# Performance work log

Hardware: AMD Instinct MI355X
Metric: run time of the kernel (lower is better)

Reference implementation:

```python
import jax, jax.numpy as jnp
import numpy as np

B, T, C = 4, 2048, 768
H, N = 12, 64
N_LAYER, LAYER_ID = 12, 1
EPS_GN = 0.00064


def setup_inputs():
    key = jax.random.key(0)
    ks = jax.random.split(key, 20)
    r01 = LAYER_ID / (N_LAYER - 1)
    r10 = 1.0 - LAYER_ID / N_LAYER
    ddd = (np.arange(C, dtype=np.float64) / C)[None, None, :]

    def lam(p, off=0.0):
        return jnp.asarray(1.0 - np.power(ddd, p) - off, dtype=jnp.float32)

    decay = -7.0 + 5.0 * (np.arange(C, dtype=np.float64) / (C - 1)) ** (0.85 + r01 ** 0.5)

    def rn(i, shape, scale):
        return scale * jax.random.normal(ks[i], shape, jnp.float32)

    s = 1.0 / C ** 0.5
    return {
        "x": jax.random.normal(ks[0], (B, T, C), jnp.float32),
        "v_first": jax.random.normal(ks[1], (B, T, C), jnp.float32),
        "lambda_r": lam(0.2 * r10), "lambda_w": lam(0.9 * r10),
        "lambda_k": lam(0.9 * r10, 0.4 * r01), "lambda_v": lam(0.4 * r10, 0.6 * r01),
        "lambda_a": lam(0.9 * r10), "lambda_g": lam(0.2 * r10),
        "w_miu": jnp.asarray(decay[None, None, :] + 0.5, jnp.float32),
        "w_A": rn(2, (C, 64), 0.02), "w_B": rn(3, (64, C), 0.02),
        "a_miu": jnp.zeros((1, 1, C), jnp.float32),
        "a_A": rn(4, (C, 64), 0.02), "a_B": rn(5, (64, C), 0.02),
        "v_miu": jnp.ones((1, 1, C), jnp.float32),
        "v_A": rn(6, (C, 64), 0.02), "v_B": rn(7, (64, C), 0.02),
        "g_A": rn(8, (C, 128), 0.02), "g_B": rn(9, (128, C), 0.02),
        "k_k": 0.85 * jnp.ones((1, 1, C), jnp.float32),
        "k_a": jnp.ones((1, 1, C), jnp.float32),
        "r_k": rn(10, (H, N), 0.02),
        "W_r": jax.random.uniform(ks[11], (C, C), jnp.float32, -0.5 * s, 0.5 * s),
        "W_k": jax.random.uniform(ks[12], (C, C), jnp.float32, -0.05 * s, 0.05 * s),
        "W_v": jax.random.uniform(ks[13], (C, C), jnp.float32, -0.5 * s, 0.5 * s),
        "W_o": rn(14, (C, C), 0.02),
        "ln_w": jnp.ones((C,), jnp.float32), "ln_b": jnp.zeros((C,), jnp.float32),
    }


def _wkv7(r, w, k, v, z, b):
    # r,w,k,v,z,b: (B,T,H,N). RWKV-7 linear recurrence with per-head NxN state:
    # S_t = S_{t-1}*diag(exp(-exp(w_t))) + (S_{t-1} z_t) b_t^T + v_t k_t^T ; y_t = S_t r_t
    decay = jnp.exp(-jnp.exp(w))

    def step(S, inp):
        rt, dt, kt, vt, zt, bt = inp  # each (B,H,N)
        sa = jnp.einsum('bhij,bhj->bhi', S, zt)
        S = S * dt[:, :, None, :] + sa[..., None] * bt[:, :, None, :] + vt[..., None] * kt[:, :, None, :]
        y = jnp.einsum('bhij,bhj->bhi', S, rt)
        return S, y

    seq = tuple(jnp.moveaxis(t, 1, 0) for t in (r, decay, k, v, z, b))  # (T,B,H,N)
    S0 = jnp.zeros((r.shape[0], r.shape[2], r.shape[3], r.shape[3]), r.dtype)
    _, ys = jax.lax.scan(step, S0, seq)
    return jnp.moveaxis(ys, 0, 1)  # (B,T,H,N)


def reference(x, v_first, lambda_r, lambda_w, lambda_k, lambda_v, lambda_a, lambda_g,
              w_miu, w_A, w_B, a_miu, a_A, a_B, v_miu, v_A, v_B, g_A, g_B,
              k_k, k_a, r_k, W_r, W_k, W_v, W_o, ln_w, ln_b):
    Bb, Tt, Cc = x.shape
    # ZeroPad2d((0,0,1,-1)): shift sequence right by 1, zero at t=0
    x_shift = jnp.pad(x, ((0, 0), (1, 0), (0, 0)))[:, :-1]
    xd = x_shift - x
    r = (x + xd * lambda_r) @ W_r.T
    w = x + xd * lambda_w
    k = (x + xd * lambda_k) @ W_k.T
    v = (x + xd * lambda_v) @ W_v.T
    a_in = x + xd * lambda_a
    g_in = x + xd * lambda_g
    if LAYER_ID == 0:
        v_first = v
    else:
        v = v + (v_first - v) * jax.nn.sigmoid(v_miu + (v @ v_A) @ v_B)
    w = -jax.nn.softplus(-(w_miu + jnp.tanh(w @ w_A) @ w_B)) - 0.5
    a = jax.nn.sigmoid(a_miu + (a_in @ a_A) @ a_B)
    g = jax.nn.sigmoid(g_in @ g_A) @ g_B
    kk = (k * k_k).reshape(Bb, Tt, H, N)
    kk = kk / jnp.maximum(jnp.linalg.norm(kk, axis=-1, keepdims=True), 1e-12)
    k = k * (1 + (a - 1) * k_a)
    rh = r.reshape(Bb, Tt, H, N)
    wh = w.reshape(Bb, Tt, H, N)
    kh = k.reshape(Bb, Tt, H, N)
    vh = v.reshape(Bb, Tt, H, N)
    ah = a.reshape(Bb, Tt, H, N)
    y = _wkv7(rh, wh, kh, vh, -kk, kk * ah)  # (B,T,H,N)
    # GroupNorm over heads, eps=0.00064, biased variance (torch semantics)
    mu = y.mean(-1, keepdims=True)
    var = y.var(-1, keepdims=True)
    y = ((y - mu) / jnp.sqrt(var + EPS_GN)).reshape(Bb, Tt, Cc) * ln_w + ln_b
    y = y + ((rh * kh * r_k).sum(-1, keepdims=True) * vh).reshape(Bb, Tt, Cc)
    out = (y * g) @ W_o.T
    return (out, v_first)
```

## Files before the change

kernel.cpp:

```cpp
#include <hip/hip_runtime.h>
#include <hip/hip_bf16.h>
#include <math.h>


#define B_  4
#define T_  2048
#define C_  768
#define H_  12

typedef __attribute__((ext_vector_type(8))) short bf16x8;
typedef __attribute__((ext_vector_type(4))) float f32x4;

#define GLD16(gsrc, ldst)                                                     \
  __builtin_amdgcn_global_load_lds(                                           \
      (const __attribute__((address_space(1))) void*)(gsrc),                  \
      (__attribute__((address_space(3))) void*)(ldst), 16, 0, 0)

template <int CTRL>
static __device__ __forceinline__ float row_ror_add(float v) {
  int t = __builtin_amdgcn_update_dpp(0, __float_as_int(v), CTRL, 0xF, 0xF, true);
  return v + __int_as_float(t);
}
static __device__ __forceinline__ float row_sum16(float v) {
  v = row_ror_add<0x128>(v);
  v = row_ror_add<0x124>(v);
  v = row_ror_add<0x122>(v);
  v = row_ror_add<0x121>(v);
  return v;
}
static __device__ __forceinline__ float wave_sum64(float v) {
  v = row_sum16(v);
  v += __shfl_xor(v, 16);
  v += __shfl_xor(v, 32);
  return v;
}

static __device__ __forceinline__ short bf16b(float f) {
  __hip_bfloat16 h = __float2bfloat16(f);
  return *reinterpret_cast<short*>(&h);
}
static __device__ __forceinline__ float bf2f(short s) {
  const unsigned u = ((unsigned)(unsigned short)s) << 16;
  return __int_as_float((int)u);
}

enum { EPI_NONE = 0, EPI_TANH, EPI_WDECAY, EPI_SIGBIAS, EPI_SIGMOID, EPI_VMIX };

static __device__ __forceinline__ float apply_epi_f(int epi, float val, int n,
                                                    int gmrow, int N,
                                                    const float* bias,
                                                    const float* ex1,
                                                    const float* ex2) {
  if (epi == EPI_TANH) {
    val = tanhf(val);
  } else if (epi == EPI_WDECAY) {
    const float u = bias[n] + val;
    const float sig = 1.f / (1.f + expf(-u));
    val = expf(-0.60653065971263342f * sig);
  } else if (epi == EPI_SIGBIAS) {
    const float u = bias[n] + val;
    val = 1.f / (1.f + expf(-u));
  } else if (epi == EPI_SIGMOID) {
    val = 1.f / (1.f + expf(-val));
  } else if (epi == EPI_VMIX) {
    const float u = bias[n] + val;
    const float sg = 1.f / (1.f + expf(-u));
    const size_t off = (size_t)gmrow * N + n;
    const float v0v = ex1[off];
    const float vf = ex2[off];
    val = v0v + (vf - v0v) * sg;
  }
  return val;
}

static __device__ __forceinline__ void gemm128_tile(
    const short* __restrict__ A, const short* __restrict__ Bw,
    float* __restrict__ C, short* __restrict__ C16, int M, int N, int K,
    int bx, int by, int epi, const float* bias, const float* ex1,
    const float* ex2, short* As, short* Bs) {
  const int tid = threadIdx.x;
  const int wave = tid >> 6, lane = tid & 63;
  const int m0 = by * 128, n0 = bx * 128;
  const int wm = (wave >> 1) * 64, wn = (wave & 1) * 64;
  const int fr = lane & 15, fk = (lane >> 4) * 8;

  f32x4 acc[4][4];
#pragma unroll
  for (int i = 0; i < 4; i++)
#pragma unroll
    for (int j = 0; j < 4; j++) acc[i][j] = (f32x4){0.f, 0.f, 0.f, 0.f};

  const int srow = tid >> 2, scol = (tid & 3) * 8;
  const short* gA = A + (size_t)(m0 + srow) * K + scol;
  const short* gB = Bw + (size_t)(n0 + srow) * K + scol;
  short* lA0 = &As[wave * 512];
  short* lA1 = &As[2048 + wave * 512];
  short* lB0 = &Bs[wave * 512];
  short* lB1 = &Bs[2048 + wave * 512];

  for (int k0 = 0; k0 < K; k0 += 32) {
    GLD16(gA + k0, lA0);
    GLD16(gA + (size_t)64 * K + k0, lA1);
    GLD16(gB + k0, lB0);
    GLD16(gB + (size_t)64 * K + k0, lB1);
    __syncthreads();

    bf16x8 af[4], bf[4];
#pragma unroll
    for (int i = 0; i < 4; i++)
      af[i] = *(const bf16x8*)&As[(wm + i * 16 + fr) * 32 + fk];
#pragma unroll
    for (int j = 0; j < 4; j++)
      bf[j] = *(const bf16x8*)&Bs[(wn + j * 16 + fr) * 32 + fk];
#pragma unroll
    for (int i = 0; i < 4; i++)
#pragma unroll
      for (int j = 0; j < 4; j++)
        acc[i][j] =
            __builtin_amdgcn_mfma_f32_16x16x32_bf16(af[i], bf[j], acc[i][j], 0, 0, 0);
    __syncthreads();
  }

#pragma unroll
  for (int i = 0; i < 4; i++) {
    const int gm = m0 + wm + i * 16 + (lane >> 4) * 4;
#pragma unroll
    for (int j = 0; j < 4; j++) {
      const int gn = n0 + wn + j * 16 + fr;
#pragma unroll
      for (int rix = 0; rix < 4; rix++) {
        float val = acc[i][j][rix];
        val = apply_epi_f(epi, val, gn, gm + rix, N, bias, ex1, ex2);
        C[(size_t)(gm + rix) * N + gn] = val;
        if (C16) C16[(size_t)(gm + rix) * N + gn] = bf16b(val);
      }
    }
  }
}

static __device__ __forceinline__ void gemm64_tile(
    const short* __restrict__ A, const short* __restrict__ Bw,
    short* __restrict__ out16, int M, int N, int K, int bx, int by, int epi,
    short* As, short* Bs) {
  const int tid = threadIdx.x;
  const int wave = tid >> 6, lane = tid & 63;
  const int m0 = by * 128, n0 = bx * 64;
  const int wm = (wave >> 1) * 64, wn = (wave & 1) * 32;
  const int fr = lane & 15, fk = (lane >> 4) * 8;

  f32x4 acc[4][2];
#pragma unroll
  for (int i = 0; i < 4; i++)
#pragma unroll
    for (int j = 0; j < 2; j++) acc[i][j] = (f32x4){0.f, 0.f, 0.f, 0.f};

  const int srow = tid >> 2, scol = (tid & 3) * 8;
  const short* gA = A + (size_t)(m0 + srow) * K + scol;
  const short* gB = Bw + (size_t)(n0 + srow) * K + scol;
  short* lA0 = &As[wave * 512];
  short* lA1 = &As[2048 + wave * 512];
  short* lB0 = &Bs[wave * 512];

  for (int k0 = 0; k0 < K; k0 += 32) {
    GLD16(gA + k0, lA0);
    GLD16(gA + (size_t)64 * K + k0, lA1);
    GLD16(gB + k0, lB0);
    __syncthreads();

    bf16x8 af[4], bf[2];
#pragma unroll
    for (int i = 0; i < 4; i++)
      af[i] = *(const bf16x8*)&As[(wm + i * 16 + fr) * 32 + fk];
#pragma unroll
    for (int j = 0; j < 2; j++)
      bf[j] = *(const bf16x8*)&Bs[(wn + j * 16 + fr) * 32 + fk];
#pragma unroll
    for (int i = 0; i < 4; i++)
#pragma unroll
      for (int j = 0; j < 2; j++)
        acc[i][j] =
            __builtin_amdgcn_mfma_f32_16x16x32_bf16(af[i], bf[j], acc[i][j], 0, 0, 0);
    __syncthreads();
  }

#pragma unroll
  for (int i = 0; i < 4; i++) {
    const int gm = m0 + wm + i * 16 + (lane >> 4) * 4;
#pragma unroll
    for (int j = 0; j < 2; j++) {
      const int gn = n0 + wn + j * 16 + fr;
#pragma unroll
      for (int rix = 0; rix < 4; rix++) {
        float val = acc[i][j][rix];
        if (epi == EPI_TANH) val = tanhf(val);
        else if (epi == EPI_SIGMOID) val = 1.f / (1.f + expf(-val));
        out16[(size_t)(gm + rix) * N + gn] = bf16b(val);
      }
    }
  }
}

__global__ __launch_bounds__(256) void big3_k(
    const short* __restrict__ xr, const short* __restrict__ xk,
    const short* __restrict__ xv, const short* __restrict__ wrb,
    const short* __restrict__ wkb, const short* __restrict__ wvb,
    float* __restrict__ r_, float* __restrict__ kbuf,
    float* __restrict__ vbuf, short* __restrict__ vbuf16) {
  __shared__ short smem[2 * 128 * 32];
  const int role = blockIdx.x / 6, bx = blockIdx.x % 6;
  const short* A;
  const short* Bw;
  float* C;
  short* C16 = nullptr;
  if (role == 0) { A = xr; Bw = wrb; C = r_; }
  else if (role == 1) { A = xk; Bw = wkb; C = kbuf; }
  else { A = xv; Bw = wvb; C = vbuf; C16 = vbuf16; }
  gemm128_tile(A, Bw, C, C16, B_ * T_, C_, C_, bx, blockIdx.y, EPI_NONE,
               nullptr, nullptr, nullptr, smem, smem + 128 * 32);
}

__global__ __launch_bounds__(256) void s1x4_k(
    const short* __restrict__ xw, const short* __restrict__ xa,
    const short* __restrict__ xg, const short* __restrict__ vbuf16,
    const short* __restrict__ wAT, const short* __restrict__ aAT,
    const short* __restrict__ gAT, const short* __restrict__ vAT,
    short* __restrict__ h_w, short* __restrict__ h_a,
    short* __restrict__ h_g, short* __restrict__ h_v) {
  __shared__ short smem[128 * 32 + 64 * 32];
  const int bx = blockIdx.x;
  const short* A;
  const short* Bw;
  short* O;
  int N, tb, epi;
  if (bx == 0)      { A = xw;     Bw = wAT; O = h_w; N = 64;  tb = 0; epi = EPI_TANH; }
  else if (bx == 1) { A = xa;     Bw = aAT; O = h_a; N = 64;  tb = 0; epi = EPI_NONE; }
  else if (bx == 2) { A = xg;     Bw = gAT; O = h_g; N = 128; tb = 0; epi = EPI_SIGMOID; }
  else if (bx == 3) { A = xg;     Bw = gAT; O = h_g; N = 128; tb = 1; epi = EPI_SIGMOID; }
  else              { A = vbuf16; Bw = vAT; O = h_v; N = 64;  tb = 0; epi = EPI_NONE; }
  gemm64_tile(A, Bw, O, B_ * T_, N, C_, tb, blockIdx.y, epi, smem,
              smem + 128 * 32);
}

__global__ __launch_bounds__(256) void s2x3_k(
    const short* __restrict__ h_v, const short* __restrict__ h_w,
    const short* __restrict__ h_a, const short* __restrict__ vBT,
    const short* __restrict__ wBT, const short* __restrict__ aBT,
    float* __restrict__ vbuf, float* __restrict__ dec_, float* __restrict__ a_,
    const float* __restrict__ v_miu, const float* __restrict__ w_miu,
    const float* __restrict__ a_miu, const float* __restrict__ v_first) {
  __shared__ short smem[2 * 128 * 32];
  const int role = blockIdx.x / 6, bx = blockIdx.x % 6;
  const short* A;
  const short* Bw;
  float* C;
  const float* bias;
  const float* ex1 = nullptr;
  const float* ex2 = nullptr;
  int epi;
  if (role == 0) { A = h_v; Bw = vBT; C = vbuf; bias = v_miu; ex1 = vbuf; ex2 = v_first; epi = EPI_VMIX; }
  else if (role == 1) { A = h_w; Bw = wBT; C = dec_; bias = w_miu; epi = EPI_WDECAY; }
  else { A = h_a; Bw = aBT; C = a_; bias = a_miu; epi = EPI_SIGBIAS; }
  gemm128_tile(A, Bw, C, nullptr, B_ * T_, C_, 64, bx, blockIdx.y, epi, bias,
               ex1, ex2, smem, smem + 128 * 32);
}

__global__ __launch_bounds__(256) void outp_k(
    const short* __restrict__ ymb, const short* __restrict__ wob,
    float* __restrict__ out) {
  __shared__ short smem[2 * 128 * 32];
  gemm128_tile(ymb, wob, out, nullptr, B_ * T_, C_, C_, blockIdx.x,
               blockIdx.y, EPI_NONE, nullptr, nullptr, nullptr, smem,
               smem + 128 * 32);
}

__global__ __launch_bounds__(256) void mix6_k(
    const float* __restrict__ x, const float* __restrict__ lr,
    const float* __restrict__ lk, const float* __restrict__ lv,
    const float* __restrict__ lw, const float* __restrict__ la,
    const float* __restrict__ lg, short* __restrict__ xr,
    short* __restrict__ xk, short* __restrict__ xv, short* __restrict__ xw,
    short* __restrict__ xa, short* __restrict__ xg) {
  const int i = blockIdx.x * 256 + threadIdx.x;
  const int c4 = i % (C_ / 4);
  const int gm = i / (C_ / 4);
  const float4 xa4 = ((const float4*)x)[i];
  float4 xp = make_float4(0.f, 0.f, 0.f, 0.f);
  if ((gm % T_) != 0) xp = ((const float4*)x)[i - C_ / 4];
  const float4 dx =
      make_float4(xp.x - xa4.x, xp.y - xa4.y, xp.z - xa4.z, xp.w - xa4.w);

#define MIXOUT(dst, lam)                                                      \
  {                                                                           \
    const float4 l4 = ((const float4*)lam)[c4];                               \
    short4 o = {bf16b(fmaf(dx.x, l4.x, xa4.x)),                               \
                bf16b(fmaf(dx.y, l4.y, xa4.y)),                               \
                bf16b(fmaf(dx.z, l4.z, xa4.z)),                               \
                bf16b(fmaf(dx.w, l4.w, xa4.w))};                              \
    ((short4*)dst)[i] = o;                                                    \
  }
  MIXOUT(xr, lr);
  MIXOUT(xk, lk);
  MIXOUT(xv, lv);
  MIXOUT(xw, lw);
  MIXOUT(xa, la);
  MIXOUT(xg, lg);
#undef MIXOUT
}

__global__ __launch_bounds__(256) void wprep_k(
    const float* __restrict__ W_r, const float* __restrict__ W_k,
    const float* __restrict__ W_v, const float* __restrict__ W_o,
    const float* __restrict__ w_A, const float* __restrict__ a_A,
    const float* __restrict__ v_A, const float* __restrict__ g_A,
    const float* __restrict__ w_B, const float* __restrict__ a_B,
    const float* __restrict__ v_B, const float* __restrict__ g_B,
    short* __restrict__ wrb, short* __restrict__ wkb,
    short* __restrict__ wvb, short* __restrict__ wob,
    short* __restrict__ wAT, short* __restrict__ aAT,
    short* __restrict__ vAT, short* __restrict__ gAT,
    short* __restrict__ wBT, short* __restrict__ aBT,
    short* __restrict__ vBT, short* __restrict__ gBT) {
  const int job = blockIdx.y;
  const int WN = C_ * C_;
  if (job < 4) {
    const float* src = (job == 0) ? W_r : (job == 1) ? W_k : (job == 2) ? W_v : W_o;
    short* dst = (job == 0) ? wrb : (job == 1) ? wkb : (job == 2) ? wvb : wob;
    const int n4 = WN / 4;
    for (int i = blockIdx.x * 256 + threadIdx.x; i < n4; i += gridDim.x * 256) {
      const float4 v = ((const float4*)src)[i];
      short4 o = {bf16b(v.x), bf16b(v.y), bf16b(v.z), bf16b(v.w)};
      ((short4*)dst)[i] = o;
    }
  } else {
    const float* in;
    short* out;
    int R, Cc;
    switch (job) {
      case 4: in = w_A; out = wAT; R = C_; Cc = 64; break;
      case 5: in = a_A; out = aAT; R = C_; Cc = 64; break;
      case 6: in = v_A; out = vAT; R = C_; Cc = 64; break;
      case 7: in = g_A; out = gAT; R = C_; Cc = 128; break;
      case 8: in = w_B; out = wBT; R = 64; Cc = C_; break;
      case 9: in = a_B; out = aBT; R = 64; Cc = C_; break;
      case 10: in = v_B; out = vBT; R = 64; Cc = C_; break;
      default: in = g_B; out = gBT; R = 128; Cc = C_; break;
    }
    const int n = R * Cc;
    for (int i = blockIdx.x * 256 + threadIdx.x; i < n; i += gridDim.x * 256) {
      const int r = i / Cc, c = i % Cc;
      out[(size_t)c * R + r] = bf16b(in[i]);
    }
  }
}

__global__ __launch_bounds__(256) void kkprep_k(
    const float* __restrict__ k0, const float* __restrict__ av_,
    const float* __restrict__ rr, const float* __restrict__ k_k,
    const float* __restrict__ k_a, float* __restrict__ kout,
    short* __restrict__ zb16, short* __restrict__ kr16) {
  const int tid = threadIdx.x;
  const int wv = tid >> 6, l = tid & 63;
  const int grp = l >> 4, g16 = l & 15;
  const size_t hid = (size_t)blockIdx.x * 16 + wv * 4 + grp;
  const int h = (int)(hid % H_);
  const size_t base = hid * 64 + g16 * 4;
  const int cc = h * 64 + g16 * 4;

  const float4 kv = *(const float4*)(k0 + base);
  const float4 aa = *(const float4*)(av_ + base);
  const float4 rv = *(const float4*)(rr + base);
  const float4 kkc = *(const float4*)(k_k + cc);
  const float4 kac = *(const float4*)(k_a + cc);

  const float kkx = kv.x * kkc.x, kky = kv.y * kkc.y, kkz = kv.z * kkc.z,
              kkw = kv.w * kkc.w;
  const float ssp = kkx * kkx + kky * kky + kkz * kkz + kkw * kkw;
  const float ss = row_sum16(ssp);
  const float denom = fmaxf(sqrtf(ss), 1e-12f);
  const float nx = kkx / denom, ny = kky / denom, nz = kkz / denom,
              nw = kkw / denom;

  bf16x8 zb = {bf16b(-nx), bf16b(-ny), bf16b(-nz), bf16b(-nw),
               bf16b(nx * aa.x), bf16b(ny * aa.y), bf16b(nz * aa.z),
               bf16b(nw * aa.w)};
  *(bf16x8*)(zb16 + hid * 128 + g16 * 8) = zb;

  const float knx = kv.x * (1.f + (aa.x - 1.f) * kac.x);
  const float kny = kv.y * (1.f + (aa.y - 1.f) * kac.y);
  const float knz = kv.z * (1.f + (aa.z - 1.f) * kac.z);
  const float knw = kv.w * (1.f + (aa.w - 1.f) * kac.w);
  bf16x8 kr = {bf16b(knx), bf16b(kny), bf16b(knz), bf16b(knw),
               bf16b(rv.x), bf16b(rv.y), bf16b(rv.z), bf16b(rv.w)};
  *(bf16x8*)(kr16 + hid * 128 + g16 * 8) = kr;

  *(float4*)(kout + base) = make_float4(knx, kny, knz, knw);
}

#define CH 16
#define NC (T_ / CH)
__global__ __launch_bounds__(256, 1) void wkv7f_k(
    const float* __restrict__ dd, const float* __restrict__ vv,
    const short* __restrict__ zb16, const short* __restrict__ kr16,
    float* __restrict__ yy, const short* __restrict__ h_g,
    const short* __restrict__ gBT, float* __restrict__ g_,
    const float4* __restrict__ cpsrc, float4* __restrict__ cpdst, int n4) {
  __shared__ __align__(16) char smem[2 * 16384];
  const int blk = blockIdx.x;

  if (blk >= 240) {
    const int rb = blk - 240;
    for (int i = rb * 256 + threadIdx.x; i < n4; i += 16 * 256)
      cpdst[i] = cpsrc[i];
    return;
  }
  if (blk >= 192) {
    short* As = (short*)smem;
    short* Bs = As + 128 * 32;
    const int rb = blk - 192;
    for (int it = 0; it < 8; ++it) {
      const int tile = rb + it * 48;
      gemm128_tile(h_g, gBT, g_, nullptr, B_ * T_, C_, 128, tile % 6,
                   tile / 6, EPI_NONE, nullptr, nullptr, nullptr, As, Bs);
    }
    return;
  }

  const int bh = blk % 48;
  const int rq = blk / 48;
  const int b = bh / H_, h = bh % H_;
  const int tid = threadIdx.x;
  const int wave = tid >> 6;
  const int l = tid & 63;
  const int l16 = l & 15;
  const int row = rq * 16 + wave * 4 + (l >> 4);
  const int cb = l16 * 4;
  const size_t btb = (size_t)b * T_;

  const size_t gf0 = (btb + wave * 4 + (l >> 4)) * C_ + h * 64 + cb;
  const size_t gp0 =
      ((btb + wave * 4 + (l >> 4)) * H_ + h) * 128 + (size_t)(l & 15) * 8;

#define STAGE(BUF, GF, GP)                                                    \
  {                                                                           \
    char* Bb = smem + (BUF)*16384;                                            \
    GLD16(dd + (GF), (float*)Bb + wave * 256);                                \
    GLD16(vv + (GF), (float*)(Bb + 4096) + wave * 256);                       \
    GLD16(zb16 + (GP), (short*)(Bb + 8192) + wave * 512);                     \
    GLD16(kr16 + (GP), (short*)(Bb + 12288) + wave * 512);                    \
  }

#define CHUNK_BODY(BUFOFF, CIDX)                                              \
  {                                                                           \
    const float* Lw = (const float*)(smem + (BUFOFF));                        \
    const float* Lv = (const float*)(smem + (BUFOFF) + 4096);                 \
    const short* Lzb = (const short*)(smem + (BUFOFF) + 8192);                \
    const short* Lkr = (const short*)(smem + (BUFOFF) + 12288);               \
    float4 Wf[CH];                                                            \
    float Vf[CH];                                                             \
    bf16x8 ZB[CH], KR[CH];                                                    \
    _Pragma("unroll") for (int j = 0; j < CH; ++j) {                          \
      Wf[j] = *(const float4*)&Lw[j * 64 + cb];                               \
      Vf[j] = Lv[j * 64 + row];                                               \
      ZB[j] = *(const bf16x8*)&Lzb[j * 128 + l16 * 8];                        \
      KR[j] = *(const bf16x8*)&Lkr[j * 128 + l16 * 8];                        \
    }                                                                         \
    _Pragma("unroll") for (int tl = 0; tl < CH; ++tl) {                       \
      const float4 w4 = Wf[tl];                                               \
      const float vi = Vf[tl];                                                \
      const bf16x8 zb = ZB[tl], kr = KR[tl];                                  \
      const float z0 = bf2f(zb[0]), z1 = bf2f(zb[1]), z2 = bf2f(zb[2]),       \
                  z3 = bf2f(zb[3]);                                           \
      const float b0 = bf2f(zb[4]), b1 = bf2f(zb[5]), b2 = bf2f(zb[6]),       \
                  b3 = bf2f(zb[7]);                                           \
      const float k0 = bf2f(kr[0]), k1 = bf2f(kr[1]), k2 = bf2f(kr[2]),       \
                  k3 = bf2f(kr[3]);                                           \
      const float r0 = bf2f(kr[4]), r1 = bf2f(kr[5]), r2 = bf2f(kr[6]),       \
                  r3 = bf2f(kr[7]);                                           \
      float sa = fmaf(S1, z1, S0 * z0) + fmaf(S3, z3, S2 * z2);               \
      sa = row_sum16(sa);                                                     \
      S0 = fmaf(S0, w4.x, fmaf(sa, b0, vi * k0));                             \
      S1 = fmaf(S1, w4.y, fmaf(sa, b1, vi * k1));                             \
      S2 = fmaf(S2, w4.z, fmaf(sa, b2, vi * k2));                             \
      S3 = fmaf(S3, w4.w, fmaf(sa, b3, vi * k3));                             \
      float yp = fmaf(S1, r1, S0 * r0) + fmaf(S3, r3, S2 * r2);               \
      yp = row_sum16(yp);                                                     \
      if (l16 == 0) yy[ybase + (size_t)((CIDX)*CH + tl) * C_] = yp;           \
    }                                                                         \
  }

  STAGE(0, gf0, gp0);
  __syncthreads();

  float S0 = 0.f, S1 = 0.f, S2 = 0.f, S3 = 0.f;
  size_t gf = gf0 + (size_t)CH * C_;
  size_t gp = gp0 + (size_t)CH * H_ * 128;
  const size_t ybase = btb * C_ + h * 64 + row;

  for (int c = 0; c < NC; c += 2) {
    STAGE(1, gf, gp);
    gf += (size_t)CH * C_;
    gp += (size_t)CH * H_ * 128;
    CHUNK_BODY(0, c)
    __syncthreads();
    if (c + 2 < NC) STAGE(0, gf, gp);
    gf += (size_t)CH * C_;
    gp += (size_t)CH * H_ * 128;
    CHUNK_BODY(16384, c + 1)
    __syncthreads();
  }
#undef STAGE
#undef CHUNK_BODY
}

__global__ __launch_bounds__(256) void gn_k(
    const float* __restrict__ y, const float* __restrict__ r,
    const float* __restrict__ k, const float* __restrict__ v,
    const float* __restrict__ g, const float* __restrict__ r_k,
    const float* __restrict__ ln_w, const float* __restrict__ ln_b,
    short* __restrict__ ymb) {
  const int tid = threadIdx.x;
  const int wv = tid >> 6, l = tid & 63;
  const int grp = l >> 4, g16 = l & 15;
  const size_t hid = (size_t)blockIdx.x * 16 + wv * 4 + grp;
  const int h = (int)(hid % H_);
  const size_t base = hid * 64 + g16 * 4;
  const int cc = h * 64 + g16 * 4;

  const float4 y4 = *(const float4*)(y + base);
  const float4 r4 = *(const float4*)(r + base);
  const float4 k4 = *(const float4*)(k + base);
  const float4 v4 = *(const float4*)(v + base);
  const float4 g4 = *(const float4*)(g + base);
  const float4 rk4 = *(const float4*)(r_k + cc);
  const float4 lw4 = *(const float4*)(ln_w + cc);
  const float4 lb4 = *(const float4*)(ln_b + cc);

  const float mu =
      row_sum16(y4.x + y4.y + y4.z + y4.w) * (1.f / 64.f);
  const float sq =
      row_sum16(y4.x * y4.x + y4.y * y4.y + y4.z * y4.z + y4.w * y4.w) *
      (1.f / 64.f);
  const float s = row_sum16(r4.x * k4.x * rk4.x + r4.y * k4.y * rk4.y +
                            r4.z * k4.z * rk4.z + r4.w * k4.w * rk4.w);
  const float inv = rsqrtf(sq - mu * mu + 0.00064f);

  short4 o;
  o.x = bf16b((fmaf((y4.x - mu) * inv, lw4.x, fmaf(s, v4.x, lb4.x))) * g4.x);
  o.y = bf16b((fmaf((y4.y - mu) * inv, lw4.y, fmaf(s, v4.y, lb4.y))) * g4.y);
  o.z = bf16b((fmaf((y4.z - mu) * inv, lw4.z, fmaf(s, v4.z, lb4.z))) * g4.z);
  o.w = bf16b((fmaf((y4.w - mu) * inv, lw4.w, fmaf(s, v4.w, lb4.w))) * g4.w);
  *(short4*)(ymb + base) = o;
}

extern "C" void kernel_launch(void* const* d_in, const int* in_sizes, int n_in,
                              void* d_out, int out_size, void* d_ws,
                              size_t ws_size, hipStream_t stream) {
  const float* x       = (const float*)d_in[0];
  const float* v_first = (const float*)d_in[1];
  const float* lam_r   = (const float*)d_in[2];
  const float* lam_w   = (const float*)d_in[3];
  const float* lam_k   = (const float*)d_in[4];
  const float* lam_v   = (const float*)d_in[5];
  const float* lam_a   = (const float*)d_in[6];
  const float* lam_g   = (const float*)d_in[7];
  const float* w_miu   = (const float*)d_in[8];
  const float* w_A     = (const float*)d_in[9];
  const float* w_B     = (const float*)d_in[10];
  const float* a_miu   = (const float*)d_in[11];
  const float* a_A     = (const float*)d_in[12];
  const float* a_B     = (const float*)d_in[13];
  const float* v_miu   = (const float*)d_in[14];
  const float* v_A     = (const float*)d_in[15];
  const float* v_B     = (const float*)d_in[16];
  const float* g_A     = (const float*)d_in[17];
  const float* g_B     = (const float*)d_in[18];
  const float* k_k     = (const float*)d_in[19];
  const float* k_a     = (const float*)d_in[20];
  const float* r_k     = (const float*)d_in[21];
  const float* W_r     = (const float*)d_in[22];
  const float* W_k     = (const float*)d_in[23];
  const float* W_v     = (const float*)d_in[24];
  const float* W_o     = (const float*)d_in[25];
  const float* ln_w    = (const float*)d_in[26];
  const float* ln_b    = (const float*)d_in[27];

  const int M = B_ * T_;
  const size_t S = (size_t)M * C_;

  float* ws   = (float*)d_ws;
  float* r_   = ws + 0 * S;
  float* kbuf = ws + 1 * S;
  float* vbuf = ws + 2 * S;
  float* dec_ = ws + 3 * S;
  float* a_   = ws + 4 * S;
  float* g_   = ws + 5 * S;
  float* z_   = ws + 6 * S;
  float* bb_  = ws + 7 * S;
  float* h_   = ws + 8 * S;
  short* wb   = (short*)(h_ + (size_t)M * 128);
  float* out  = (float*)d_out;

  const int WN = C_ * C_;
  short* wrb = wb + 0 * (size_t)WN;
  short* wkb = wb + 1 * (size_t)WN;
  short* wvb = wb + 2 * (size_t)WN;
  short* wob = wb + 3 * (size_t)WN;
  short* wAT = wb + 4 * (size_t)WN;
  short* aAT = wAT + (size_t)C_ * 64;
  short* vAT = aAT + (size_t)C_ * 64;
  short* gAT = vAT + (size_t)C_ * 64;
  short* wBT = gAT + (size_t)C_ * 128;
  short* aBT = wBT + (size_t)C_ * 64;
  short* vBT = aBT + (size_t)C_ * 64;
  short* gBT = vBT + (size_t)C_ * 64;

  short* xr  = (short*)dec_;
  short* xk  = (short*)a_;
  short* xv  = (short*)g_;
  short* xw  = (short*)z_;
  short* xa  = (short*)z_ + S;
  short* xg  = (short*)bb_;
  short* vbuf16 = (short*)bb_ + S;
  short* h_w = (short*)h_;
  short* h_a = h_w + (size_t)M * 64;
  short* h_g = h_a + (size_t)M * 64;
  short* h_v = (short*)g_;
  short* zb16 = (short*)z_;
  short* kr16 = (short*)bb_;
  short* ymb = (short*)z_;

  {
    dim3 blk(256), grid(576, 12);
    hipLaunchKernelGGL(wprep_k, grid, blk, 0, stream, W_r, W_k, W_v, W_o,
                       w_A, a_A, v_A, g_A, w_B, a_B, v_B, g_B, wrb, wkb, wvb,
                       wob, wAT, aAT, vAT, gAT, wBT, aBT, vBT, gBT);
  }
  {
    dim3 blk(256), grid((int)(S / 4 / 256));
    hipLaunchKernelGGL(mix6_k, grid, blk, 0, stream, x, lam_r, lam_k, lam_v,
                       lam_w, lam_a, lam_g, xr, xk, xv, xw, xa, xg);
  }
  {
    dim3 blk(256), grid(18, M / 128);
    hipLaunchKernelGGL(big3_k, grid, blk, 0, stream, xr, xk, xv, wrb, wkb,
                       wvb, r_, kbuf, vbuf, vbuf16);
  }
  {
    dim3 blk(256), grid(5, M / 128);
    hipLaunchKernelGGL(s1x4_k, grid, blk, 0, stream, xw, xa, xg, vbuf16, wAT,
                       aAT, gAT, vAT, h_w, h_a, h_g, h_v);
  }
  {
    dim3 blk(256), grid(18, M / 128);
    hipLaunchKernelGGL(s2x3_k, grid, blk, 0, stream, h_v, h_w, h_a, vBT, wBT,
                       aBT, vbuf, dec_, a_, v_miu, w_miu, a_miu, v_first);
  }
  {
    dim3 grid((B_ * T_ * H_) / 16), blk(256);
    hipLaunchKernelGGL(kkprep_k, grid, blk, 0, stream, kbuf, a_, r_, k_k,
                       k_a, kbuf, zb16, kr16);
  }
  {
    dim3 grid(256), blk(256);
    hipLaunchKernelGGL(wkv7f_k, grid, blk, 0, stream, dec_, vbuf, zb16, kr16,
                       a_, h_g, gBT, g_, (const float4*)v_first,
                       (float4*)(out + S), (int)(S / 4));
  }
  {
    dim3 grid((B_ * T_ * H_) / 16), blk(256);
    hipLaunchKernelGGL(gn_k, grid, blk, 0, stream, a_, r_, kbuf, vbuf, g_, r_k,
                       ln_w, ln_b, ymb);
  }
  {
    dim3 blk(256), grid(C_ / 128, M / 128);
    hipLaunchKernelGGL(outp_k, grid, blk, 0, stream, ymb, wob, out);
  }
}
```

Baseline: 760.2 us.

## Split WKV state rows across four times more blocks with interleaved bf16 operands

```diff
diff --git a/kernel.cpp b/kernel.cpp
--- a/kernel.cpp
+++ b/kernel.cpp
@@ -38,10 +38,6 @@
 static __device__ __forceinline__ short bf16b(float f) {
   __hip_bfloat16 h = __float2bfloat16(f);
   return *reinterpret_cast<short*>(&h);
-}
-static __device__ __forceinline__ float bf2f(short s) {
-  const unsigned u = ((unsigned)(unsigned short)s) << 16;
-  return __int_as_float((int)u);
 }
 
 enum { EPI_NONE = 0, EPI_TANH, EPI_WDECAY, EPI_SIGBIAS, EPI_SIGMOID, EPI_VMIX };
@@ -357,7 +353,7 @@
     const float* __restrict__ k0, const float* __restrict__ av_,
     const float* __restrict__ rr, const float* __restrict__ k_k,
     const float* __restrict__ k_a, float* __restrict__ kout,
-    short* __restrict__ zb16, short* __restrict__ kr16) {
+    short* __restrict__ zbkr) {
   const int tid = threadIdx.x;
   const int wv = tid >> 6, l = tid & 63;
   const int grp = l >> 4, g16 = l & 15;
@@ -380,43 +376,42 @@
   const float nx = kkx / denom, ny = kky / denom, nz = kkz / denom,
               nw = kkw / denom;
 
-  bf16x8 zb = {bf16b(-nx), bf16b(-ny), bf16b(-nz), bf16b(-nw),
-               bf16b(nx * aa.x), bf16b(ny * aa.y), bf16b(nz * aa.z),
-               bf16b(nw * aa.w)};
-  *(bf16x8*)(zb16 + hid * 128 + g16 * 8) = zb;
-
   const float knx = kv.x * (1.f + (aa.x - 1.f) * kac.x);
   const float kny = kv.y * (1.f + (aa.y - 1.f) * kac.y);
   const float knz = kv.z * (1.f + (aa.z - 1.f) * kac.z);
   const float knw = kv.w * (1.f + (aa.w - 1.f) * kac.w);
-  bf16x8 kr = {bf16b(knx), bf16b(kny), bf16b(knz), bf16b(knw),
-               bf16b(rv.x), bf16b(rv.y), bf16b(rv.z), bf16b(rv.w)};
-  *(bf16x8*)(kr16 + hid * 128 + g16 * 8) = kr;
+
+  bf16x8 q0 = {bf16b(-nx), bf16b(nx * aa.x), bf16b(knx), bf16b(rv.x),
+               bf16b(-ny), bf16b(ny * aa.y), bf16b(kny), bf16b(rv.y)};
+  bf16x8 q1 = {bf16b(-nz), bf16b(nz * aa.z), bf16b(knz), bf16b(rv.z),
+               bf16b(-nw), bf16b(nw * aa.w), bf16b(knw), bf16b(rv.w)};
+  *(bf16x8*)(zbkr + hid * 256 + g16 * 16) = q0;
+  *(bf16x8*)(zbkr + hid * 256 + g16 * 16 + 8) = q1;
 
   *(float4*)(kout + base) = make_float4(knx, kny, knz, knw);
 }
 
 #define CH 16
 #define NC (T_ / CH)
-__global__ __launch_bounds__(256, 1) void wkv7f_k(
+__global__ __launch_bounds__(256, 3) void wkv7f_k(
     const float* __restrict__ dd, const float* __restrict__ vv,
-    const short* __restrict__ zb16, const short* __restrict__ kr16,
-    float* __restrict__ yy, const short* __restrict__ h_g,
-    const short* __restrict__ gBT, float* __restrict__ g_,
-    const float4* __restrict__ cpsrc, float4* __restrict__ cpdst, int n4) {
+    const short* __restrict__ zbkr, float* __restrict__ yy,
+    const short* __restrict__ h_g, const short* __restrict__ gBT,
+    float* __restrict__ g_, const float4* __restrict__ cpsrc,
+    float4* __restrict__ cpdst, int n4) {
   __shared__ __align__(16) char smem[2 * 16384];
   const int blk = blockIdx.x;
 
-  if (blk >= 240) {
-    const int rb = blk - 240;
+  if (blk >= 816) {
+    const int rb = blk - 816;
     for (int i = rb * 256 + threadIdx.x; i < n4; i += 16 * 256)
       cpdst[i] = cpsrc[i];
     return;
   }
-  if (blk >= 192) {
+  if (blk >= 768) {
     short* As = (short*)smem;
     short* Bs = As + 128 * 32;
-    const int rb = blk - 192;
+    const int rb = blk - 768;
     for (int it = 0; it < 8; ++it) {
       const int tile = rb + it * 48;
       gemm128_tile(h_g, gBT, g_, nullptr, B_ * T_, C_, 128, tile % 6,
@@ -426,85 +421,57 @@
   }
 
   const int bh = blk % 48;
-  const int rq = blk / 48;
+  const int qq = blk / 48;
   const int b = bh / H_, h = bh % H_;
   const int tid = threadIdx.x;
   const int wave = tid >> 6;
-  const int l = tid & 63;
-  const int l16 = l & 15;
-  const int row = rq * 16 + wave * 4 + (l >> 4);
-  const int cb = l16 * 4;
+  const int lane = tid & 63;
+  const int row = qq * 4 + wave;
   const size_t btb = (size_t)b * T_;
 
-  const size_t gf0 = (btb + wave * 4 + (l >> 4)) * C_ + h * 64 + cb;
-  const size_t gp0 =
-      ((btb + wave * 4 + (l >> 4)) * H_ + h) * 128 + (size_t)(l & 15) * 8;
-
-#define STAGE(BUF, GF, GP)                                                    \
+#define STAGE(BUF, TCH)                                                       \
   {                                                                           \
     char* Bb = smem + (BUF)*16384;                                            \
-    GLD16(dd + (GF), (float*)Bb + wave * 256);                                \
-    GLD16(vv + (GF), (float*)(Bb + 4096) + wave * 256);                       \
-    GLD16(zb16 + (GP), (short*)(Bb + 8192) + wave * 512);                     \
-    GLD16(kr16 + (GP), (short*)(Bb + 12288) + wave * 512);                    \
+    const size_t tokA = btb + (size_t)(TCH)*CH;                               \
+    GLD16(zbkr + ((tokA + (tid >> 5)) * H_ + h) * 256 + (tid & 31) * 8,       \
+          (short*)Bb + wave * 512);                                           \
+    GLD16(zbkr + ((tokA + 8 + (tid >> 5)) * H_ + h) * 256 + (tid & 31) * 8,   \
+          (short*)(Bb + 4096) + wave * 512);                                  \
+    GLD16(dd + (tokA + (tid >> 4)) * C_ + h * 64 + (tid & 15) * 4,            \
+          (float*)(Bb + 8192) + wave * 256);                                  \
+    GLD16(vv + (tokA + (tid >> 4)) * C_ + h * 64 + (tid & 15) * 4,            \
+          (float*)(Bb + 12288) + wave * 256);                                 \
   }
 
 #define CHUNK_BODY(BUFOFF, CIDX)                                              \
   {                                                                           \
-    const float* Lw = (const float*)(smem + (BUFOFF));                        \
-    const float* Lv = (const float*)(smem + (BUFOFF) + 4096);                 \
-    const short* Lzb = (const short*)(smem + (BUFOFF) + 8192);                \
-    const short* Lkr = (const short*)(smem + (BUFOFF) + 12288);               \
-    float4 Wf[CH];                                                            \
-    float Vf[CH];                                                             \
-    bf16x8 ZB[CH], KR[CH];                                                    \
-    _Pragma("unroll") for (int j = 0; j < CH; ++j) {                          \
-      Wf[j] = *(const float4*)&Lw[j * 64 + cb];                               \
-      Vf[j] = Lv[j * 64 + row];                                               \
-      ZB[j] = *(const bf16x8*)&Lzb[j * 128 + l16 * 8];                        \
-      KR[j] = *(const bf16x8*)&Lkr[j * 128 + l16 * 8];                        \
+    const char* Lb = smem + (BUFOFF);                                         \
+    _Pragma("unroll") for (int tl = 0; tl < CH; ++tl) {                       \
+      const int2 pk = *(const int2*)(Lb + tl * 512 + lane * 8);               \
+      const float wv_ = *(const float*)(Lb + 8192 + tl * 256 + lane * 4);     \
+      const float vi = *(const float*)(Lb + 12288 + tl * 256 + row * 4);      \
+      const float z = __int_as_float(pk.x << 16);                             \
+      const float bb = __int_as_float(pk.x & 0xffff0000);                     \
+      const float k = __int_as_float(pk.y << 16);                             \
+      const float r = __int_as_float(pk.y & 0xffff0000);                      \
+      float sa = wave_sum64(S * z);                                           \
+      S = fmaf(S, wv_, fmaf(sa, bb, vi * k));                                 \
+      float yp = wave_sum64(S * r);                                           \
+      if (lane == 0) yy[ybase + (size_t)((CIDX)*CH + tl) * C_] = yp;          \
     }                                                                         \
-    _Pragma("unroll") for (int tl = 0; tl < CH; ++tl) {                       \
-      const float4 w4 = Wf[tl];                                               \
-      const float vi = Vf[tl];                                                \
-      const bf16x8 zb = ZB[tl], kr = KR[tl];                                  \
-      const float z0 = bf2f(zb[0]), z1 = bf2f(zb[1]), z2 = bf2f(zb[2]),       \
-                  z3 = bf2f(zb[3]);                                           \
-      const float b0 = bf2f(zb[4]), b1 = bf2f(zb[5]), b2 = bf2f(zb[6]),       \
-                  b3 = bf2f(zb[7]);                                           \
-      const float k0 = bf2f(kr[0]), k1 = bf2f(kr[1]), k2 = bf2f(kr[2]),       \
-                  k3 = bf2f(kr[3]);                                           \
-      const float r0 = bf2f(kr[4]), r1 = bf2f(kr[5]), r2 = bf2f(kr[6]),       \
-                  r3 = bf2f(kr[7]);                                           \
-      float sa = fmaf(S1, z1, S0 * z0) + fmaf(S3, z3, S2 * z2);               \
-      sa = row_sum16(sa);                                                     \
-      S0 = fmaf(S0, w4.x, fmaf(sa, b0, vi * k0));                             \
-      S1 = fmaf(S1, w4.y, fmaf(sa, b1, vi * k1));                             \
-      S2 = fmaf(S2, w4.z, fmaf(sa, b2, vi * k2));                             \
-      S3 = fmaf(S3, w4.w, fmaf(sa, b3, vi * k3));                             \
-      float yp = fmaf(S1, r1, S0 * r0) + fmaf(S3, r3, S2 * r2);               \
-      yp = row_sum16(yp);                                                     \
-      if (l16 == 0) yy[ybase + (size_t)((CIDX)*CH + tl) * C_] = yp;           \
-    }                                                                         \
-  }
-
-  STAGE(0, gf0, gp0);
+  }
+
+  STAGE(0, 0);
   __syncthreads();
 
-  float S0 = 0.f, S1 = 0.f, S2 = 0.f, S3 = 0.f;
-  size_t gf = gf0 + (size_t)CH * C_;
-  size_t gp = gp0 + (size_t)CH * H_ * 128;
+  float S = 0.f;
   const size_t ybase = btb * C_ + h * 64 + row;
 
   for (int c = 0; c < NC; c += 2) {
-    STAGE(1, gf, gp);
-    gf += (size_t)CH * C_;
-    gp += (size_t)CH * H_ * 128;
+    STAGE(1, c + 1);
     CHUNK_BODY(0, c)
     __syncthreads();
-    if (c + 2 < NC) STAGE(0, gf, gp);
-    gf += (size_t)CH * C_;
-    gp += (size_t)CH * H_ * 128;
+    if (c + 2 < NC) STAGE(0, c + 2);
     CHUNK_BODY(16384, c + 1)
     __syncthreads();
   }
@@ -625,8 +592,7 @@
   short* h_a = h_w + (size_t)M * 64;
   short* h_g = h_a + (size_t)M * 64;
   short* h_v = (short*)g_;
-  short* zb16 = (short*)z_;
-  short* kr16 = (short*)bb_;
+  short* zbkr = (short*)z_;
   short* ymb = (short*)z_;
 
   {
@@ -658,11 +624,11 @@
   {
     dim3 grid((B_ * T_ * H_) / 16), blk(256);
     hipLaunchKernelGGL(kkprep_k, grid, blk, 0, stream, kbuf, a_, r_, k_k,
-                       k_a, kbuf, zb16, kr16);
-  }
-  {
-    dim3 grid(256), blk(256);
-    hipLaunchKernelGGL(wkv7f_k, grid, blk, 0, stream, dec_, vbuf, zb16, kr16,
+                       k_a, kbuf, zbkr);
+  }
+  {
+    dim3 grid(832), blk(256);
+    hipLaunchKernelGGL(wkv7f_k, grid, blk, 0, stream, dec_, vbuf, zbkr,
                        a_, h_g, gBT, g_, (const float4*)v_first,
                        (float4*)(out + S), (int)(S / 4));
   }
```

Measured after the change: 1.054 ms. 38.6% more time.

## Precompute k·r and b·r dots so WKV output needs one fewer serial reduction

Applied to the files above, without the earlier changes.

```diff
diff --git a/kernel.cpp b/kernel.cpp
--- a/kernel.cpp
+++ b/kernel.cpp
@@ -357,7 +357,8 @@
     const float* __restrict__ k0, const float* __restrict__ av_,
     const float* __restrict__ rr, const float* __restrict__ k_k,
     const float* __restrict__ k_a, float* __restrict__ kout,
-    short* __restrict__ zb16, short* __restrict__ kr16) {
+    short* __restrict__ zb16, short* __restrict__ kr16,
+    float* __restrict__ dots) {
   const int tid = threadIdx.x;
   const int wv = tid >> 6, l = tid & 63;
   const int grp = l >> 4, g16 = l & 15;
@@ -394,17 +395,36 @@
   *(bf16x8*)(kr16 + hid * 128 + g16 * 8) = kr;
 
   *(float4*)(kout + base) = make_float4(knx, kny, knz, knw);
+
+  float p3 = 0.f, p4 = 0.f;
+#pragma unroll
+  for (int j = 0; j < 4; j++) {
+    const float rj = bf2f(kr[j + 4]);
+    p3 = fmaf(bf2f(kr[j]), rj, p3);
+    p4 = fmaf(bf2f(zb[j + 4]), rj, p4);
+  }
+  const float d3 = row_sum16(p3);
+  const float d4 = row_sum16(p4);
+  if (g16 == 0) {
+    const size_t th = hid / H_;
+    const size_t b = th / T_, t = th % T_;
+    const size_t di = ((b * H_ + h) * T_ + t) * 2;
+    dots[di] = d3;
+    dots[di + 1] = d4;
+  }
 }
 
 #define CH 16
 #define NC (T_ / CH)
-__global__ __launch_bounds__(256, 1) void wkv7f_k(
+#define BUFSZ 17408
+__global__ __launch_bounds__(256) void wkv7f_k(
     const float* __restrict__ dd, const float* __restrict__ vv,
     const short* __restrict__ zb16, const short* __restrict__ kr16,
-    float* __restrict__ yy, const short* __restrict__ h_g,
-    const short* __restrict__ gBT, float* __restrict__ g_,
-    const float4* __restrict__ cpsrc, float4* __restrict__ cpdst, int n4) {
-  __shared__ __align__(16) char smem[2 * 16384];
+    const float* __restrict__ dots, float* __restrict__ yy,
+    const short* __restrict__ h_g, const short* __restrict__ gBT,
+    float* __restrict__ g_, const float4* __restrict__ cpsrc,
+    float4* __restrict__ cpdst, int n4) {
+  __shared__ __align__(16) char smem[2 * BUFSZ];
   const int blk = blockIdx.x;
 
   if (blk >= 240) {
@@ -439,14 +459,25 @@
   const size_t gf0 = (btb + wave * 4 + (l >> 4)) * C_ + h * 64 + cb;
   const size_t gp0 =
       ((btb + wave * 4 + (l >> 4)) * H_ + h) * 128 + (size_t)(l & 15) * 8;
-
-#define STAGE(BUF, GF, GP)                                                    \
+  const size_t gd0 = (size_t)bh * T_ * 2;
+
+#define STAGE(BUF, GF, GP, GD)                                                \
   {                                                                           \
-    char* Bb = smem + (BUF)*16384;                                            \
+    char* Bb = smem + (BUF)*BUFSZ;                                            \
     GLD16(dd + (GF), (float*)Bb + wave * 256);                                \
     GLD16(vv + (GF), (float*)(Bb + 4096) + wave * 256);                       \
     GLD16(zb16 + (GP), (short*)(Bb + 8192) + wave * 512);                     \
     GLD16(kr16 + (GP), (short*)(Bb + 12288) + wave * 512);                    \
+    if (wave == 0) GLD16(dots + (GD) + (size_t)l * 4, (float*)(Bb + 16384));  \
+  }
+
+#define LDSTEP(S_, TL_)                                                       \
+  {                                                                           \
+    Wf[S_] = *(const float4*)&Lw[(TL_)*64 + cb];                              \
+    Vf[S_] = Lv[(TL_)*64 + row];                                              \
+    ZB[S_] = *(const bf16x8*)&Lzb[(TL_)*128 + l16 * 8];                       \
+    KR[S_] = *(const bf16x8*)&Lkr[(TL_)*128 + l16 * 8];                       \
+    DT[S_] = *(const float2*)&Ldt[(TL_)*2];                                   \
   }
 
 #define CHUNK_BODY(BUFOFF, CIDX)                                              \
@@ -455,19 +486,20 @@
     const float* Lv = (const float*)(smem + (BUFOFF) + 4096);                 \
     const short* Lzb = (const short*)(smem + (BUFOFF) + 8192);                \
     const short* Lkr = (const short*)(smem + (BUFOFF) + 12288);               \
-    float4 Wf[CH];                                                            \
-    float Vf[CH];                                                             \
-    bf16x8 ZB[CH], KR[CH];                                                    \
-    _Pragma("unroll") for (int j = 0; j < CH; ++j) {                          \
-      Wf[j] = *(const float4*)&Lw[j * 64 + cb];                               \
-      Vf[j] = Lv[j * 64 + row];                                               \
-      ZB[j] = *(const bf16x8*)&Lzb[j * 128 + l16 * 8];                        \
-      KR[j] = *(const bf16x8*)&Lkr[j * 128 + l16 * 8];                        \
-    }                                                                         \
+    const float* Ldt = (const float*)(smem + (BUFOFF) + 16384);               \
+    float4 Wf[3];                                                             \
+    float Vf[3];                                                              \
+    float2 DT[3];                                                             \
+    bf16x8 ZB[3], KR[3];                                                      \
+    LDSTEP(0, 0);                                                             \
+    LDSTEP(1, 1);                                                             \
     _Pragma("unroll") for (int tl = 0; tl < CH; ++tl) {                       \
-      const float4 w4 = Wf[tl];                                               \
-      const float vi = Vf[tl];                                                \
-      const bf16x8 zb = ZB[tl], kr = KR[tl];                                  \
+      const int sl = tl % 3;                                                  \
+      if (tl + 2 < CH) { LDSTEP((tl + 2) % 3, tl + 2); }                      \
+      const float4 w4 = Wf[sl];                                               \
+      const float vi = Vf[sl];                                                \
+      const float2 dt = DT[sl];                                               \
+      const bf16x8 zb = ZB[sl], kr = KR[sl];                                  \
       const float z0 = bf2f(zb[0]), z1 = bf2f(zb[1]), z2 = bf2f(zb[2]),       \
                   z3 = bf2f(zb[3]);                                           \
       const float b0 = bf2f(zb[4]), b1 = bf2f(zb[5]), b2 = bf2f(zb[6]),       \
@@ -476,39 +508,46 @@
                   k3 = bf2f(kr[3]);                                           \
       const float r0 = bf2f(kr[4]), r1 = bf2f(kr[5]), r2 = bf2f(kr[6]),       \
                   r3 = bf2f(kr[7]);                                           \
-      float sa = fmaf(S1, z1, S0 * z0) + fmaf(S3, z3, S2 * z2);               \
-      sa = row_sum16(sa);                                                     \
+                     \
+      float sa_p = fmaf(S1, z1, S0 * z0) + fmaf(S3, z3, S2 * z2);             \
+      float yw_p = fmaf(S1, w4.y * r1, S0 * (w4.x * r0)) +                    \
+                   fmaf(S3, w4.w * r3, S2 * (w4.z * r2));                     \
+      const float sa = row_sum16(sa_p);                                       \
+      const float yw = row_sum16(yw_p);                                       \
       S0 = fmaf(S0, w4.x, fmaf(sa, b0, vi * k0));                             \
       S1 = fmaf(S1, w4.y, fmaf(sa, b1, vi * k1));                             \
       S2 = fmaf(S2, w4.z, fmaf(sa, b2, vi * k2));                             \
       S3 = fmaf(S3, w4.w, fmaf(sa, b3, vi * k3));                             \
-      float yp = fmaf(S1, r1, S0 * r0) + fmaf(S3, r3, S2 * r2);               \
-      yp = row_sum16(yp);                                                     \
+      const float yp = fmaf(sa, dt.y, fmaf(vi, dt.x, yw));                    \
       if (l16 == 0) yy[ybase + (size_t)((CIDX)*CH + tl) * C_] = yp;           \
     }                                                                         \
   }
 
-  STAGE(0, gf0, gp0);
+  STAGE(0, gf0, gp0, gd0);
   __syncthreads();
 
   float S0 = 0.f, S1 = 0.f, S2 = 0.f, S3 = 0.f;
   size_t gf = gf0 + (size_t)CH * C_;
   size_t gp = gp0 + (size_t)CH * H_ * 128;
+  size_t gd = gd0 + (size_t)CH * 2;
   const size_t ybase = btb * C_ + h * 64 + row;
 
   for (int c = 0; c < NC; c += 2) {
-    STAGE(1, gf, gp);
+    STAGE(1, gf, gp, gd);
     gf += (size_t)CH * C_;
     gp += (size_t)CH * H_ * 128;
+    gd += (size_t)CH * 2;
     CHUNK_BODY(0, c)
     __syncthreads();
-    if (c + 2 < NC) STAGE(0, gf, gp);
+    if (c + 2 < NC) STAGE(0, gf, gp, gd);
     gf += (size_t)CH * C_;
     gp += (size_t)CH * H_ * 128;
-    CHUNK_BODY(16384, c + 1)
+    gd += (size_t)CH * 2;
+    CHUNK_BODY(BUFSZ, c + 1)
     __syncthreads();
   }
 #undef STAGE
+#undef LDSTEP
 #undef CHUNK_BODY
 }
 
@@ -613,6 +652,8 @@
   short* aBT = wBT + (size_t)C_ * 64;
   short* vBT = aBT + (size_t)C_ * 64;
   short* gBT = vBT + (size_t)C_ * 64;
+  short* wend = gBT + (size_t)C_ * 128;
+  float* dots = (float*)((((uintptr_t)wend) + 15) & ~(uintptr_t)15);
 
   short* xr  = (short*)dec_;
   short* xk  = (short*)a_;
@@ -658,12 +699,12 @@
   {
     dim3 grid((B_ * T_ * H_) / 16), blk(256);
     hipLaunchKernelGGL(kkprep_k, grid, blk, 0, stream, kbuf, a_, r_, k_k,
-                       k_a, kbuf, zb16, kr16);
+                       k_a, kbuf, zb16, kr16, dots);
   }
   {
     dim3 grid(256), blk(256);
     hipLaunchKernelGGL(wkv7f_k, grid, blk, 0, stream, dec_, vbuf, zb16, kr16,
-                       a_, h_g, gBT, g_, (const float4*)v_first,
+                       dots, a_, h_g, gBT, g_, (const float4*)v_first,
                        (float4*)(out + S), (int)(S / 4));
   }
   {
```

Measured after the change: 758.5 us. No clear change (-0.2%).
